# Performance work log

Hardware: AMD Instinct MI355X
Metric: run time of the kernel (lower is better)

The kernel has to match this reference:

```python
import jax, jax.numpy as jnp
import numpy as np

N_NODE = 100000
N_EDGE = 1600000
D_FEAT = 64
DEPTH = 3
BASEALPHA = 1.0


def setup_inputs() -> dict:
    key = jax.random.key(0)
    k1, k2, k3 = jax.random.split(key, 3)
    x = jax.random.normal(k1, (N_NODE, D_FEAT), dtype=jnp.float32)
    edge_index = jax.random.randint(k2, (2, N_EDGE), 0, N_NODE, dtype=jnp.int64)
    edge_attr = jax.random.uniform(k3, (N_EDGE,), dtype=jnp.float32)
    # learnable polynomial coefficients, init = min(1/alpha, 1) = 1.0
    alphas = jnp.ones((DEPTH + 1,), dtype=jnp.float32)
    return {"x": x, "edge_index": edge_index, "edge_attr": edge_attr, "alphas": alphas}


def reference(x, edge_index, edge_attr, alphas):
    n = x.shape[0]
    row, col = edge_index[0], edge_index[1]
    # GCN symmetric degree normalization: val_e = d_row^-1/2 * w_e * d_col^-1/2
    deg = jax.ops.segment_sum(edge_attr, row, num_segments=n)
    safe_deg = jnp.where(deg > 0, deg, 1.0)
    dinv = jnp.where(deg > 0, jax.lax.rsqrt(safe_deg), 0.0)
    val = dinv[row] * edge_attr * dinv[col]  # [E]

    a = BASEALPHA * jnp.tanh(alphas)  # [depth+1]

    def spmm(h):  # (adj @ h): out[i] = sum_{e: row_e=i} val_e * h[col_e]
        return jax.ops.segment_sum(val[:, None] * h[col], row, num_segments=n)

    # PowerConv recurrence: x_0 = x; x_L = a_L * (adj @ x_{L-1})
    xs = [x]
    for L in range(1, DEPTH + 1):
        xs.append(a[L] * spmm(xs[-1]))
    return jnp.stack(xs, axis=1)  # [N, depth+1, d]
```

## Files before the change

kernel.cpp:

```cpp
#include <hip/hip_runtime.h>
#include <math.h>

#define N_NODE 100000
#define N_EDGE 1600000
#define D_FEAT 64
#define DEPTH  3
#define OUT_STRIDE ((DEPTH + 1) * D_FEAT)

#define NB  256
#define RPB 391
#define CAP 8192
#define S1_BS 512
#define S1_CHUNK 8192
#define S1_BLOCKS ((N_EDGE + S1_CHUNK - 1) / S1_CHUNK)

#define NOCT 16
#define OCT_DIV 6250
#define NCELL (RPB * NOCT)
#define NCHUNK (NCELL / 8)

#define SPMM_NPB 16
#define SPMM_BLOCKS (N_NODE / SPMM_NPB)

#define DEG_SCALE 33554432.0f

typedef float  f32x4 __attribute__((ext_vector_type(4)));

__device__ __forceinline__ unsigned int bf16_rne(float f) {
    unsigned int u = __float_as_uint(f);
    return (u + 0x7FFFu + ((u >> 16) & 1u)) >> 16;
}

__global__ __launch_bounds__(S1_BS) void stage1_bucket(
        const int* __restrict__ ei, const float* __restrict__ ea,
        int* __restrict__ bucket_cursor, int2* __restrict__ bucket) {
    __shared__ int hist[NB];
    __shared__ int segb[NB];
    int tid = threadIdx.x;
    int e0 = blockIdx.x * S1_CHUNK;

    for (int i = tid; i < NB; i += S1_BS) hist[i] = 0;
    __syncthreads();

    for (int k = 0; k < S1_CHUNK; k += S1_BS) {
        int e = e0 + k + tid;
        if (e < N_EDGE) {
            int r = ei[e];
            atomicAdd(&hist[r / RPB], 1);
        }
    }
    __syncthreads();

    for (int i = tid; i < NB; i += S1_BS) {
        int h = hist[i];
        segb[i] = (h > 0) ? atomicAdd(&bucket_cursor[i], h) : 0;
        hist[i] = 0;
    }
    __syncthreads();

    for (int k = 0; k < S1_CHUNK; k += S1_BS) {
        int e = e0 + k + tid;
        if (e < N_EDGE) {
            int r  = ei[e];
            int b  = r / RPB;
            int rl = r - b * RPB;
            int c  = ei[N_EDGE + e];
            float w = ea[e];
            int lofs = atomicAdd(&hist[b], 1);
            int pos  = segb[b] + lofs;
            if (pos < CAP)
                bucket[(size_t)b * CAP + pos] =
                    make_int2((rl << 17) | c, __float_as_int(w));
        }
    }
}

__global__ void bucket_scan_kernel(const int* __restrict__ bucket_cursor,
                                   int* __restrict__ bucket_base,
                                   const float* __restrict__ alphas,
                                   float* __restrict__ a_vals) {
    __shared__ int sc[NB];
    int tid = threadIdx.x;
    int v = bucket_cursor[tid];
    sc[tid] = v;
    __syncthreads();
    for (int off = 1; off < NB; off <<= 1) {
        int t = (tid >= off) ? sc[tid - off] : 0;
        __syncthreads();
        sc[tid] += t;
        __syncthreads();
    }
    bucket_base[tid] = sc[tid] - v;
    if (tid < DEPTH + 1) a_vals[tid] = tanhf(alphas[tid]);
}

__global__ __launch_bounds__(1024) void stage2_fused(
        const int2* __restrict__ bucket, const int* __restrict__ bucket_cnt,
        const int* __restrict__ bucket_base,
        int* __restrict__ row_ptr, int* __restrict__ row_end,
        float* __restrict__ dinv, int2* __restrict__ csr) {
    __shared__ int          cnt2[NCELL];
    __shared__ unsigned int wdeg[RPB];
    __shared__ int          sc[1024];
    __shared__ int2         staged[CAP];
    int b = blockIdx.x, tid = threadIdx.x;

    for (int i = tid; i < NCELL; i += 1024) cnt2[i] = 0;
    if (tid < RPB) wdeg[tid] = 0u;
    __syncthreads();

    int cnt = bucket_cnt[b];
    const int2* src = bucket + (size_t)b * CAP;

    for (int i = tid; i < cnt; i += 1024) {
        int2 e = src[i];
        int rl = e.x >> 17;
        int c  = e.x & 0x1FFFF;
        int oc = c / OCT_DIV;
        atomicAdd(&cnt2[rl * NOCT + oc], 1);
        atomicAdd(&wdeg[rl],
                  (unsigned int)(__int_as_float(e.y) * DEG_SCALE + 0.5f));
    }
    __syncthreads();

    int lsum = 0;
    if (tid < NCHUNK) {
        int base = tid * 8;
        #pragma unroll
        for (int j = 0; j < 8; ++j) lsum += cnt2[base + j];
    }
    sc[tid] = lsum;
    __syncthreads();
    for (int off = 1; off < 1024; off <<= 1) {
        int t = (tid >= off) ? sc[tid - off] : 0;
        __syncthreads();
        sc[tid] += t;
        __syncthreads();
    }
    if (tid < NCHUNK) {
        int run = sc[tid] - lsum;
        int base = tid * 8;
        #pragma unroll
        for (int j = 0; j < 8; ++j) {
            int v = cnt2[base + j];
            cnt2[base + j] = run;
            run += v;
        }
    }
    __syncthreads();

    int base_b = bucket_base[b];
    if (tid < RPB) {
        int row = b * RPB + tid;
        if (row < N_NODE) {
            int rb = cnt2[tid * NOCT];
            int re = (tid == RPB - 1) ? cnt : cnt2[(tid + 1) * NOCT];
            row_ptr[row] = base_b + rb;
            row_end[row] = base_b + re;
            float d = (float)wdeg[tid] * (1.0f / DEG_SCALE);
            dinv[row] = (d > 0.0f) ? rsqrtf(d) : 0.0f;
        }
    }
    __syncthreads();

    for (int i = tid; i < cnt; i += 1024) {
        int2 e = src[i];
        int rl = e.x >> 17;
        int c  = e.x & 0x1FFFF;
        int oc = c / OCT_DIV;
        int pos = atomicAdd(&cnt2[rl * NOCT + oc], 1);
        staged[pos] = make_int2(c, e.y);
    }
    __syncthreads();

    for (int i = tid; i < cnt; i += 1024) csr[base_b + i] = staged[i];
}

__global__ void init_out_kernel(const float* __restrict__ x,
                                const float* __restrict__ dinv,
                                float* __restrict__ out,
                                unsigned short* __restrict__ hb0,
                                int write_hb) {
    int i = blockIdx.x * blockDim.x + threadIdx.x;
    if (i < N_NODE * (D_FEAT / 4)) {
        int n  = i >> 4;
        int d4 = (i & 15) << 2;
        float4 v = *(const float4*)&x[(size_t)n * D_FEAT + d4];
        f32x4 vv = {v.x, v.y, v.z, v.w};
        __builtin_nontemporal_store(
            vv, (f32x4*)&out[(size_t)n * OUT_STRIDE + d4]);
        if (write_hb) {
            float s = dinv[n];
            uint2 o;
            o.x = bf16_rne(v.x * s) | (bf16_rne(v.y * s) << 16);
            o.y = bf16_rne(v.z * s) | (bf16_rne(v.w * s) << 16);
            *(uint2*)&hb0[(size_t)n * D_FEAT + d4] = o;
        }
    }
}

__global__ __launch_bounds__(256) void spmm_bf16_kernel(
        const int* __restrict__ row_ptr,
        const int* __restrict__ row_end,
        const int2* __restrict__ csr,
        const float* __restrict__ a_vals,
        const float* __restrict__ dinv,
        const unsigned short* __restrict__ hsrc,
        unsigned short* __restrict__ hdst,
        float* __restrict__ out,
        int L, int write_hdst) {
    int wid  = threadIdx.x >> 6;
    int lane = threadIdx.x & 63;
    int grp  = lane >> 4;
    int l16  = lane & 15;
    int node = blockIdx.x * SPMM_NPB + wid * 4 + grp;
    unsigned int fo = (unsigned int)(l16 << 2);

    int beg = row_ptr[node];
    int end = row_end[node];

    float acc0 = 0.0f, acc1 = 0.0f, acc2 = 0.0f, acc3 = 0.0f;

    for (int chunk = beg; chunk < end; chunk += 16) {
        int idx = chunk + l16;
        int2 pv = (idx < end) ? csr[idx] : make_int2(0, 0);
        int navail = end - chunk;
        if (navail > 16) navail = 16;
        for (int t = 0; t < navail; t += 4) {
            #pragma unroll
            for (int k = 0; k < 4; ++k) {
                int sub = t + k;
                int   cc = __shfl(pv.x, sub, 16);
                float vv = __int_as_float(__shfl(pv.y, sub, 16));
                float w  = (sub < navail) ? vv : 0.0f;
                unsigned int off = ((unsigned int)cc << 6) + fo;
                uint2 hv = *(const uint2*)&hsrc[off];
                acc0 += w * __uint_as_float((hv.x & 0xFFFFu) << 16);
                acc1 += w * __uint_as_float(hv.x & 0xFFFF0000u);
                acc2 += w * __uint_as_float((hv.y & 0xFFFFu) << 16);
                acc3 += w * __uint_as_float(hv.y & 0xFFFF0000u);
            }
        }
    }

    float di = dinv[node];
    float aL = a_vals[L];
    float s1 = aL * di;
    float s2 = s1 * di;
    f32x4 r = {s1 * acc0, s1 * acc1, s1 * acc2, s1 * acc3};
    __builtin_nontemporal_store(
        r, (f32x4*)&out[(size_t)node * OUT_STRIDE + L * D_FEAT + fo]);
    if (write_hdst) {
        uint2 o;
        o.x = bf16_rne(s2 * acc0) | (bf16_rne(s2 * acc1) << 16);
        o.y = bf16_rne(s2 * acc2) | (bf16_rne(s2 * acc3) << 16);
        *(uint2*)&hdst[(size_t)node * D_FEAT + fo] = o;
    }
}

__global__ void spmm_f32_kernel(const int* __restrict__ row_ptr,
                                const int* __restrict__ row_end,
                                const int2* __restrict__ csr,
                                const float* __restrict__ a_vals,
                                const float* __restrict__ dinv,
                                float* __restrict__ out,
                                int L) {
    int node = blockIdx.x * (blockDim.x >> 6) + (threadIdx.x >> 6);
    int lane = threadIdx.x & 63;
    if (node >= N_NODE) return;
    int beg = row_ptr[node];
    int end = row_end[node];
    int g = lane >> 4;
    int q = lane & 15;
    int src_base = (L - 1) * D_FEAT + (q << 2);

    float4 acc = make_float4(0.0f, 0.0f, 0.0f, 0.0f);
    for (int chunk = beg; chunk < end; chunk += 64) {
        int idx = chunk + lane;
        int2 pv = (idx < end) ? csr[idx] : make_int2(0, 0);
        int navail = end - chunk;
        if (navail > 64) navail = 64;
        for (int t = 0; t < navail; t += 4) {
            int sub = t + g;
            int   cc = __shfl(pv.x, sub);
            float vv = __int_as_float(__shfl(pv.y, sub));
            bool valid = (sub < navail);
            int   c_safe = valid ? cc : 0;
            float v_safe = valid ? (vv * dinv[c_safe]) : 0.0f;
            const float4 hv =
                *(const float4*)&out[(size_t)c_safe * OUT_STRIDE + src_base];
            acc.x += v_safe * hv.x;
            acc.y += v_safe * hv.y;
            acc.z += v_safe * hv.z;
            acc.w += v_safe * hv.w;
        }
    }
    acc.x += __shfl_down(acc.x, 32);
    acc.y += __shfl_down(acc.y, 32);
    acc.z += __shfl_down(acc.z, 32);
    acc.w += __shfl_down(acc.w, 32);
    acc.x += __shfl_down(acc.x, 16);
    acc.y += __shfl_down(acc.y, 16);
    acc.z += __shfl_down(acc.z, 16);
    acc.w += __shfl_down(acc.w, 16);
    if (g == 0) {
        float s1 = a_vals[L] * dinv[node];
        float4 r = make_float4(s1 * acc.x, s1 * acc.y, s1 * acc.z, s1 * acc.w);
        *(float4*)&out[(size_t)node * OUT_STRIDE + L * D_FEAT + (q << 2)] = r;
    }
}

extern "C" void kernel_launch(void* const* d_in, const int* in_sizes, int n_in,
                              void* d_out, int out_size, void* d_ws, size_t ws_size,
                              hipStream_t stream) {
    const float* x      = (const float*)d_in[0];
    const int*   ei     = (const int*)d_in[1];
    const float* ea     = (const float*)d_in[2];
    const float* alphas = (const float*)d_in[3];
    float*       out    = (float*)d_out;

    int2*  csr          = (int2*)d_ws;
    int*   row_ptr      = (int*)(csr + N_EDGE);
    int*   row_end      = row_ptr + N_NODE;
    float* dinv         = (float*)(row_end + N_NODE);
    int*   bucket_cursor= (int*)(dinv + N_NODE);
    int*   bucket_base  = bucket_cursor + NB;
    float* a_vals       = (float*)(bucket_base + NB);
    int2*  bucket       = (int2*)(a_vals + 4);
    unsigned short* hb0 = (unsigned short*)bucket;
    unsigned short* hb1 = hb0 + (size_t)N_NODE * D_FEAT;

    size_t base_bytes = (size_t)((char*)bucket - (char*)d_ws);
    size_t need_bf16  = base_bytes +
        2 * (size_t)N_NODE * D_FEAT * sizeof(unsigned short);
    int use_bf16 = (ws_size >= need_bf16) ? 1 : 0;

    hipMemsetAsync(bucket_cursor, 0, NB * sizeof(int), stream);

    stage1_bucket<<<S1_BLOCKS, S1_BS, 0, stream>>>(ei, ea, bucket_cursor, bucket);
    bucket_scan_kernel<<<1, NB, 0, stream>>>(bucket_cursor, bucket_base,
                                             alphas, a_vals);
    stage2_fused<<<NB, 1024, 0, stream>>>(bucket, bucket_cursor, bucket_base,
                                          row_ptr, row_end, dinv, csr);
    init_out_kernel<<<(N_NODE * (D_FEAT / 4) + 255) / 256, 256, 0, stream>>>(
        x, dinv, out, hb0, use_bf16);

    if (use_bf16) {
        spmm_bf16_kernel<<<SPMM_BLOCKS, 256, 0, stream>>>(row_ptr, row_end, csr,
            a_vals, dinv, hb0, hb1, out, 1, 1);
        spmm_bf16_kernel<<<SPMM_BLOCKS, 256, 0, stream>>>(row_ptr, row_end, csr,
            a_vals, dinv, hb1, hb0, out, 2, 1);
        spmm_bf16_kernel<<<SPMM_BLOCKS, 256, 0, stream>>>(row_ptr, row_end, csr,
            a_vals, dinv, hb0, hb1, out, 3, 0);
    } else {
        int nodes_per_block = 256 / 64;
        int spmm_blocks = (N_NODE + nodes_per_block - 1) / nodes_per_block;
        for (int L = 1; L <= DEPTH; ++L) {
            spmm_f32_kernel<<<spmm_blocks, 256, 0, stream>>>(row_ptr, row_end, csr,
                a_vals, dinv, out, L);
        }
    }
}
```

Measured before the change: 322.4 us.

## Fuse bucket scan and output init into CSR build, drop column sub-sort

Removes the separate bucket scan kernel by having every stage2 block redo the prefix scan over bucket counts, and folds the x copy into out plus the dinv-scaled bf16 init of hb0 into stage2, using a shared-memory dinv. Buckets go to 512 with 196 rows each, so smaller shared staging allows more blocks. The per-row sort of columns into octants is dropped, so edges within a row are no longer grouped by column range, which may hurt gather locality in the SpMM passes. hb0 now gets its own workspace region instead of aliasing the bucket buffer, which needs more workspace.

```diff
diff --git a/kernel.cpp b/kernel.cpp
--- a/kernel.cpp
+++ b/kernel.cpp
@@ -7,17 +7,12 @@
 #define DEPTH  3
 #define OUT_STRIDE ((DEPTH + 1) * D_FEAT)
 
-#define NB  256
-#define RPB 391
-#define CAP 8192
+#define NB  512
+#define RPB 196
+#define CAP 4096
 #define S1_BS 512
 #define S1_CHUNK 8192
 #define S1_BLOCKS ((N_EDGE + S1_CHUNK - 1) / S1_CHUNK)
-
-#define NOCT 16
-#define OCT_DIV 6250
-#define NCELL (RPB * NOCT)
-#define NCHUNK (NCELL / 8)
 
 #define SPMM_NPB 16
 #define SPMM_BLOCKS (N_NODE / SPMM_NPB)
@@ -75,128 +70,103 @@
     }
 }
 
-__global__ void bucket_scan_kernel(const int* __restrict__ bucket_cursor,
-                                   int* __restrict__ bucket_base,
-                                   const float* __restrict__ alphas,
-                                   float* __restrict__ a_vals) {
-    __shared__ int sc[NB];
-    int tid = threadIdx.x;
-    int v = bucket_cursor[tid];
-    sc[tid] = v;
-    __syncthreads();
-    for (int off = 1; off < NB; off <<= 1) {
-        int t = (tid >= off) ? sc[tid - off] : 0;
-        __syncthreads();
-        sc[tid] += t;
-        __syncthreads();
-    }
-    bucket_base[tid] = sc[tid] - v;
-    if (tid < DEPTH + 1) a_vals[tid] = tanhf(alphas[tid]);
-}
-
 __global__ __launch_bounds__(1024) void stage2_fused(
         const int2* __restrict__ bucket, const int* __restrict__ bucket_cnt,
-        const int* __restrict__ bucket_base,
+        const float* __restrict__ x, const float* __restrict__ alphas,
         int* __restrict__ row_ptr, int* __restrict__ row_end,
-        float* __restrict__ dinv, int2* __restrict__ csr) {
-    __shared__ int          cnt2[NCELL];
+        float* __restrict__ dinv_g, float* __restrict__ a_vals,
+        int2* __restrict__ csr, float* __restrict__ out,
+        unsigned short* __restrict__ hb0, int write_hb) {
+    __shared__ int          bscan[NB];
+    __shared__ int          rcnt[RPB];
     __shared__ unsigned int wdeg[RPB];
-    __shared__ int          sc[1024];
+    __shared__ float        dinvl[RPB];
+    __shared__ int          lcur[RPB];
+    __shared__ int          sc[256];
     __shared__ int2         staged[CAP];
     int b = blockIdx.x, tid = threadIdx.x;
 
-    for (int i = tid; i < NCELL; i += 1024) cnt2[i] = 0;
-    if (tid < RPB) wdeg[tid] = 0u;
-    __syncthreads();
-
-    int cnt = bucket_cnt[b];
+    if (tid < NB) bscan[tid] = bucket_cnt[tid];
+    for (int i = tid; i < RPB; i += 1024) { rcnt[i] = 0; wdeg[i] = 0u; }
+    __syncthreads();
+    for (int off = 1; off < NB; off <<= 1) {
+        int t = (tid < NB && tid >= off) ? bscan[tid - off] : 0;
+        __syncthreads();
+        if (tid < NB) bscan[tid] += t;
+        __syncthreads();
+    }
+    int base_b = (b == 0) ? 0 : bscan[b - 1];
+    int cnt    = bscan[b] - base_b;
+    if (cnt > CAP) cnt = CAP;
+
     const int2* src = bucket + (size_t)b * CAP;
 
     for (int i = tid; i < cnt; i += 1024) {
         int2 e = src[i];
         int rl = e.x >> 17;
-        int c  = e.x & 0x1FFFF;
-        int oc = c / OCT_DIV;
-        atomicAdd(&cnt2[rl * NOCT + oc], 1);
+        atomicAdd(&rcnt[rl], 1);
         atomicAdd(&wdeg[rl],
                   (unsigned int)(__int_as_float(e.y) * DEG_SCALE + 0.5f));
     }
     __syncthreads();
 
-    int lsum = 0;
-    if (tid < NCHUNK) {
-        int base = tid * 8;
-        #pragma unroll
-        for (int j = 0; j < 8; ++j) lsum += cnt2[base + j];
-    }
-    sc[tid] = lsum;
-    __syncthreads();
-    for (int off = 1; off < 1024; off <<= 1) {
-        int t = (tid >= off) ? sc[tid - off] : 0;
+    int v = 0;
+    if (tid < 256) { v = (tid < RPB) ? rcnt[tid] : 0; sc[tid] = v; }
+    __syncthreads();
+    for (int off = 1; off < 256; off <<= 1) {
+        int t = 0;
+        if (tid < 256 && tid >= off) t = sc[tid - off];
         __syncthreads();
-        sc[tid] += t;
+        if (tid < 256) sc[tid] += t;
         __syncthreads();
     }
-    if (tid < NCHUNK) {
-        int run = sc[tid] - lsum;
-        int base = tid * 8;
-        #pragma unroll
-        for (int j = 0; j < 8; ++j) {
-            int v = cnt2[base + j];
-            cnt2[base + j] = run;
-            run += v;
-        }
-    }
-    __syncthreads();
-
-    int base_b = bucket_base[b];
+
     if (tid < RPB) {
+        int excl = sc[tid] - v;
+        lcur[tid] = excl;
         int row = b * RPB + tid;
+        float di = 0.0f;
         if (row < N_NODE) {
-            int rb = cnt2[tid * NOCT];
-            int re = (tid == RPB - 1) ? cnt : cnt2[(tid + 1) * NOCT];
-            row_ptr[row] = base_b + rb;
-            row_end[row] = base_b + re;
+            row_ptr[row] = base_b + excl;
+            row_end[row] = base_b + excl + rcnt[tid];
             float d = (float)wdeg[tid] * (1.0f / DEG_SCALE);
-            dinv[row] = (d > 0.0f) ? rsqrtf(d) : 0.0f;
-        }
+            di = (d > 0.0f) ? rsqrtf(d) : 0.0f;
+            dinv_g[row] = di;
+        }
+        dinvl[tid] = di;
     }
     __syncthreads();
 
     for (int i = tid; i < cnt; i += 1024) {
         int2 e = src[i];
         int rl = e.x >> 17;
-        int c  = e.x & 0x1FFFF;
-        int oc = c / OCT_DIV;
-        int pos = atomicAdd(&cnt2[rl * NOCT + oc], 1);
-        staged[pos] = make_int2(c, e.y);
+        int pos = atomicAdd(&lcur[rl], 1);
+        staged[pos] = make_int2(e.x & 0x1FFFF, e.y);
     }
     __syncthreads();
 
     for (int i = tid; i < cnt; i += 1024) csr[base_b + i] = staged[i];
-}
-
-__global__ void init_out_kernel(const float* __restrict__ x,
-                                const float* __restrict__ dinv,
-                                float* __restrict__ out,
-                                unsigned short* __restrict__ hb0,
-                                int write_hb) {
-    int i = blockIdx.x * blockDim.x + threadIdx.x;
-    if (i < N_NODE * (D_FEAT / 4)) {
-        int n  = i >> 4;
-        int d4 = (i & 15) << 2;
-        float4 v = *(const float4*)&x[(size_t)n * D_FEAT + d4];
-        f32x4 vv = {v.x, v.y, v.z, v.w};
-        __builtin_nontemporal_store(
-            vv, (f32x4*)&out[(size_t)n * OUT_STRIDE + d4]);
-        if (write_hb) {
-            float s = dinv[n];
-            uint2 o;
-            o.x = bf16_rne(v.x * s) | (bf16_rne(v.y * s) << 16);
-            o.y = bf16_rne(v.z * s) | (bf16_rne(v.w * s) << 16);
-            *(uint2*)&hb0[(size_t)n * D_FEAT + d4] = o;
-        }
-    }
+
+    for (int i = tid; i < RPB * 16; i += 1024) {
+        int r   = i >> 4;
+        int row = b * RPB + r;
+        if (row < N_NODE) {
+            int d4 = (i & 15) << 2;
+            float4 vx = *(const float4*)&x[(size_t)row * D_FEAT + d4];
+            f32x4 vv = {vx.x, vx.y, vx.z, vx.w};
+            __builtin_nontemporal_store(
+                vv, (f32x4*)&out[(size_t)row * OUT_STRIDE + d4]);
+            if (write_hb) {
+                float s = dinvl[r];
+                uint2 o;
+                o.x = bf16_rne(vx.x * s) | (bf16_rne(vx.y * s) << 16);
+                o.y = bf16_rne(vx.z * s) | (bf16_rne(vx.w * s) << 16);
+                *(uint2*)&hb0[(size_t)row * D_FEAT + d4] = o;
+            }
+        }
+    }
+
+    if (b == 0 && tid < DEPTH + 1) a_vals[tid] = tanhf(alphas[tid]);
 }
 
 __global__ __launch_bounds__(256) void spmm_bf16_kernel(
@@ -324,26 +294,21 @@
     int*   row_end      = row_ptr + N_NODE;
     float* dinv         = (float*)(row_end + N_NODE);
     int*   bucket_cursor= (int*)(dinv + N_NODE);
-    int*   bucket_base  = bucket_cursor + NB;
-    float* a_vals       = (float*)(bucket_base + NB);
+    float* a_vals       = (float*)(bucket_cursor + NB);
     int2*  bucket       = (int2*)(a_vals + 4);
-    unsigned short* hb0 = (unsigned short*)bucket;
+    unsigned short* hb0 = (unsigned short*)(bucket + (size_t)NB * CAP);
     unsigned short* hb1 = hb0 + (size_t)N_NODE * D_FEAT;
 
-    size_t base_bytes = (size_t)((char*)bucket - (char*)d_ws);
-    size_t need_bf16  = base_bytes +
-        2 * (size_t)N_NODE * D_FEAT * sizeof(unsigned short);
-    int use_bf16 = (ws_size >= need_bf16) ? 1 : 0;
+    size_t need = (size_t)((char*)hb1 - (char*)d_ws) +
+                  (size_t)N_NODE * D_FEAT * sizeof(unsigned short);
+    int use_bf16 = (ws_size >= need) ? 1 : 0;
 
     hipMemsetAsync(bucket_cursor, 0, NB * sizeof(int), stream);
 
     stage1_bucket<<<S1_BLOCKS, S1_BS, 0, stream>>>(ei, ea, bucket_cursor, bucket);
-    bucket_scan_kernel<<<1, NB, 0, stream>>>(bucket_cursor, bucket_base,
-                                             alphas, a_vals);
-    stage2_fused<<<NB, 1024, 0, stream>>>(bucket, bucket_cursor, bucket_base,
-                                          row_ptr, row_end, dinv, csr);
-    init_out_kernel<<<(N_NODE * (D_FEAT / 4) + 255) / 256, 256, 0, stream>>>(
-        x, dinv, out, hb0, use_bf16);
+    stage2_fused<<<NB, 1024, 0, stream>>>(bucket, bucket_cursor, x, alphas,
+                                          row_ptr, row_end, dinv, a_vals,
+                                          csr, out, hb0, use_bf16);
 
     if (use_bf16) {
         spmm_bf16_kernel<<<SPMM_BLOCKS, 256, 0, stream>>>(row_ptr, row_end, csr,
```

Measured after the change: 321.4 us. Within noise of the previous version (-0.3%).
